# Optimization experiments

Hardware: AMD Instinct MI355X
Metric: run time of the kernel (lower is better)

Reference implementation:

```python
import jax, jax.numpy as jnp
import numpy as np

WS = 8          # window_size
NH = 8          # num_heads
D = 256         # values_dim
DQK = 128       # inner_qk_dim = int(256 * 0.5)
DV = 256        # inner_v_dim (already divisible by NH)
H1, W1 = 128, 128
H2, W2 = 192, 192
N1 = (H1 // WS) * (W1 // WS)   # 256 windows
N2 = (H2 // WS) * (W2 // WS)   # 576 windows
EPS = 1e-6


def _windows(x):
    # (B, H, W, D) -> (B, Wh*Ww, ws*ws, D)
    B, Hx, Wx, Dd = x.shape
    Wh, Ww = Hx // WS, Wx // WS
    x = x.reshape(B, Wh, WS, Ww, WS, Dd).transpose(0, 1, 3, 2, 4, 5)
    return x.reshape(B, Wh * Ww, WS * WS, Dd), (Wh, Ww)


def _unwindows(x, Wh, Ww):
    # (B, Wh*Ww, ws*ws, D) -> (B, Wh*ws, Ww*ws, D)
    B, N, n, Dd = x.shape
    x = x.reshape(B, Wh, Ww, WS, WS, Dd).transpose(0, 1, 3, 2, 4, 5)
    return x.reshape(B, Wh * WS, Ww * WS, Dd)


def _rmsnorm(x, w):
    return x * jax.lax.rsqrt(jnp.mean(x * x, axis=-1, keepdims=True) + EPS) * w


def _qkv(x, W_qk, b_qk, rms_w, W_v):
    Vw, (Wh, Ww) = _windows(x)
    B, N, n, _ = Vw.shape
    avg = Vw.mean(axis=2)                                  # (B, N, D)
    qk = _rmsnorm(avg @ W_qk + b_qk, rms_w)                # (B, N, 2*DQK)
    # 'b Wh Ww (H e) -> b H (Wh Ww) e' then chunk(2, dim=-1)
    qk = qk.reshape(B, N, NH, 2 * DQK // NH).transpose(0, 2, 1, 3)  # (B, NH, N, 32)
    q, k = jnp.split(qk, 2, axis=-1)                       # each (B, NH, N, 16)
    v = Vw @ W_v                                           # (B, N, n, DV)
    ev = DV // NH
    # 'b Wh Ww n (e H) -> b H (Wh Ww) (n e)' (head index fastest-varying in channel)
    v = v.reshape(B, N, n, ev, NH).transpose(0, 4, 1, 2, 3).reshape(B, NH, N, n * ev)
    return q, k, v, (Wh, Ww)


def reference(x1, x2, W_qk, b_qk, rms_w, W_v, W_vb):
    q1, k1, v1, s1 = _qkv(x1, W_qk, b_qk, rms_w, W_v)
    q2, k2, v2, s2 = _qkv(x2, W_qk, b_qk, rms_w, W_v)
    q = jnp.concatenate([q1, q2], axis=2)   # (B, NH, N, 16)
    k = jnp.concatenate([k1, k2], axis=2)
    v = jnp.concatenate([v1, v2], axis=2)   # (B, NH, N, n*ev)

    scale = 1.0 / jnp.sqrt(jnp.asarray(DQK, dtype=q.dtype))
    scores = jnp.einsum('bhqe,bhke->bhqk', q, k) * scale   # (B, NH, N, N)
    # block-diagonal self-source mask
    src_id = jnp.concatenate([jnp.zeros((N1,), jnp.int32), jnp.ones((N2,), jnp.int32)])
    mask = src_id[:, None] == src_id[None, :]              # (N, N) True within same source
    scores = jnp.where(mask, -jnp.inf, scores)
    A = jax.nn.softmax(scores, axis=-1)

    out = jnp.einsum('bhqk,bhkf->bhqf', A, v)              # (B, NH, N, n*ev)
    B = out.shape[0]
    n = WS * WS
    ev = DV // NH
    N = N1 + N2
    # 'b H N (n e) -> b N n (e H)'
    out = out.reshape(B, NH, N, n, ev).transpose(0, 2, 3, 4, 1).reshape(B, N, n, ev * NH)
    out = out @ W_vb                                       # (B, N, n, D)

    o1 = _unwindows(out[:, :N1], H1 // WS, W1 // WS)
    o2 = _unwindows(out[:, N1:], H2 // WS, W2 // WS)
    return (o1, o2)


def setup_inputs() -> dict:
    key = jax.random.key(0)
    ks = jax.random.split(key, 6)
    return {
        'x1': jax.random.normal(ks[0], (2, H1, W1, D), jnp.float32),
        'x2': jax.random.normal(ks[1], (2, H2, W2, D), jnp.float32),
        'W_qk': jax.random.normal(ks[2], (D, 2 * DQK), jnp.float32) * 0.02,
        'b_qk': jnp.zeros((2 * DQK,), jnp.float32),
        'rms_w': jnp.ones((2 * DQK,), jnp.float32),
        'W_v': jax.random.normal(ks[3], (D, DV), jnp.float32) * 0.02,
        'W_vb': jax.random.normal(ks[4], (DV, D), jnp.float32) * 0.02,
    }
```

## Files before the change

kernel.cpp:

```cpp
#include <hip/hip_runtime.h>

typedef __attribute__((ext_vector_type(8))) short bf16x8;
typedef __attribute__((ext_vector_type(4))) float f32x4;

#define NWIN 832
#define N1_ 256
#define N2_ 576
#define O1SZ 8388608

__device__ __forceinline__ ushort f2bf(float f) {
    union { float f; unsigned u; } v; v.f = f;
    unsigned r = v.u + 0x7fffu + ((v.u >> 16) & 1u);
    return (ushort)(r >> 16);
}

__global__ __launch_bounds__(256) void k_prep(const float* __restrict__ W_qk,
        const float* __restrict__ W_v, const float* __restrict__ W_vb,
        ushort* __restrict__ WvT, ushort* __restrict__ WvbT, float* __restrict__ WqkT)
{
    int row = blockIdx.x & 255, m = blockIdx.x >> 8, t = threadIdx.x;
    if (m == 0) {
        int j = ((row & 31) << 3) | (row >> 5);
        WvT[row * 256 + t] = f2bf(W_v[t * 256 + j]);
    } else if (m == 1) {
        WvbT[row * 256 + t] = f2bf(W_vb[t * 256 + row]);
    } else {
        WqkT[row * 256 + t] = W_qk[t * 256 + row];
    }
}

__global__ __launch_bounds__(256) void k_projv(const float* __restrict__ x1, const float* __restrict__ x2,
        const ushort* __restrict__ WvT, float* __restrict__ avg, ushort* __restrict__ vattn)
{
    __shared__ __align__(16) char smem[37888];
    ushort (*a_lds)[264] = (ushort (*)[264])smem;
    float* psumF = (float*)(smem + 33792);

    int bid = blockIdx.x, b = bid / NWIN, win = bid % NWIN;
    const float* src; int Wd, base;
    if (win < N1_) { src = x1; Wd = 128; int wh = win >> 4, ww = win & 15;
                     base = ((b*128 + wh*8)*128 + ww*8)*256; }
    else           { src = x2; Wd = 192; int w2 = win - N1_; int wh = w2/24, ww = w2%24;
                     base = ((b*192 + wh*8)*192 + ww*8)*256; }

    int t = threadIdx.x;
    int c4 = t & 63, tg = t >> 6;
    int c0 = c4 * 4;
    const float* sp = src + base + c0;
    float4 s4 = {0.f, 0.f, 0.f, 0.f};
    #pragma unroll
    for (int k = 0; k < 16; ++k) {
        int i = tg*16 + k;
        float4 g = *(const float4*)(sp + ((i>>3)*Wd + (i&7))*256);
        s4.x += g.x; s4.y += g.y; s4.z += g.z; s4.w += g.w;
        ushort4 hb = { f2bf(g.x), f2bf(g.y), f2bf(g.z), f2bf(g.w) };
        *(ushort4*)&a_lds[i][c0] = hb;
    }
    *(float4*)&psumF[tg*256 + c0] = s4;
    __syncthreads();

    {
        float a = psumF[t] + psumF[256 + t] + psumF[512 + t] + psumF[768 + t];
        avg[(b*NWIN + win)*256 + t] = a * 0.015625f;
    }

    int lane = t & 63, wv = t >> 6, lr = lane & 15, lg = lane >> 4;
    f32x4 acc[4][4];
    #pragma unroll
    for (int mt=0;mt<4;++mt)
      #pragma unroll
      for (int nt=0;nt<4;++nt) acc[mt][nt] = (f32x4){0.f,0.f,0.f,0.f};

    #pragma unroll 2
    for (int ks = 0; ks < 8; ++ks) {
        bf16x8 af[4], bfr[4];
        #pragma unroll
        for (int mt=0;mt<4;++mt) af[mt] = *(const bf16x8*)&a_lds[mt*16 + lr][ks*32 + lg*8];
        #pragma unroll
        for (int nt=0;nt<4;++nt) bfr[nt] = *(const bf16x8*)&WvT[(wv*64 + nt*16 + lr)*256 + ks*32 + lg*8];
        #pragma unroll
        for (int mt=0;mt<4;++mt)
          #pragma unroll
          for (int nt=0;nt<4;++nt)
            acc[mt][nt] = __builtin_amdgcn_mfma_f32_16x16x32_bf16(af[mt], bfr[nt], acc[mt][nt], 0, 0, 0);
    }

    __syncthreads();
    ushort (*sw)[72] = (ushort (*)[72])(smem + wv*9216);

    #pragma unroll
    for (int nt=0; nt<4; ++nt) {
        int c = nt*16 + lr;
        #pragma unroll
        for (int mt=0; mt<4; ++mt) {
            ushort4 hb = { f2bf(acc[mt][nt][0]), f2bf(acc[mt][nt][1]),
                           f2bf(acc[mt][nt][2]), f2bf(acc[mt][nt][3]) };
            *(ushort4*)&sw[c][mt*16 + lg*4] = hb;
        }
    }
    #pragma unroll
    for (int u=0; u<2; ++u) {
        int h = wv*2 + u;
        ushort* dst = &vattn[((size_t)(b*8 + h)*NWIN + win)*2048];
        #pragma unroll
        for (int it=0; it<4; ++it) {
            int q = it*64 + lane;
            int e = q >> 3, i8 = (q & 7) * 8;
            *(uint4*)&dst[e*64 + i8] = *(const uint4*)&sw[u*32 + e][i8];
        }
    }
}

__global__ __launch_bounds__(256) void k_qk(const float* __restrict__ avg, const float* __restrict__ WqkT,
        const float* __restrict__ b_qk, const float* __restrict__ rms_w,
        float* __restrict__ qv, float* __restrict__ kv)
{
    __shared__ float arow[256];
    __shared__ float red[256];
    int row = blockIdx.x, c = threadIdx.x;
    arow[c] = avg[row*256 + c];
    __syncthreads();
    const float4* wr = (const float4*)&WqkT[c*256];
    float t = 0.f;
    #pragma unroll 8
    for (int k4 = 0; k4 < 64; ++k4) {
        float4 w = wr[k4];
        t += arow[k4*4]*w.x + arow[k4*4+1]*w.y + arow[k4*4+2]*w.z + arow[k4*4+3]*w.w;
    }
    t += b_qk[c];
    red[c] = t*t;
    __syncthreads();
    for (int s = 128; s; s >>= 1) { if (c < s) red[c] += red[c+s]; __syncthreads(); }
    float ms = red[0] * (1.f/256.f);
    float y = t * rsqrtf(ms + 1e-6f) * rms_w[c];
    int b = row / NWIN, win = row % NWIN;
    int h = c >> 5, sub = c & 31;
    size_t ob = ((size_t)(b*8 + h)*NWIN + win)*16 + (sub & 15);
    if (sub < 16) qv[ob] = y; else kv[ob] = y;
}

__global__ __launch_bounds__(256) void k_sm(const float* __restrict__ qv, const float* __restrict__ kv,
        ushort* __restrict__ Amat)
{
    __shared__ float red[256];
    int rowid = blockIdx.x;
    int qg = rowid % NWIN, bh = rowid / NWIN;
    bool s1 = qg < N1_;
    int Nk = s1 ? N2_ : N1_;
    int kbase = s1 ? N1_ : 0;
    size_t Abase = (size_t)bh*294912 + (s1 ? (size_t)qg*576 : (147456 + (size_t)(qg - N1_)*256));
    const float4* qp = (const float4*)&qv[((size_t)bh*NWIN + qg)*16];
    float4 q0 = qp[0], q1 = qp[1], q2 = qp[2], q3 = qp[3];
    const float* kp = &kv[((size_t)bh*NWIN + kbase)*16];
    int t = threadIdx.x;
    float sc[3];
    #pragma unroll
    for (int it = 0; it < 3; ++it) {
        int kk = t + it*256;
        sc[it] = -1e30f;
        if (kk < Nk) {
            const float4* kr = (const float4*)&kp[(size_t)kk*16];
            float4 a = kr[0], bq = kr[1], cq = kr[2], dq = kr[3];
            float d = q0.x*a.x + q0.y*a.y + q0.z*a.z + q0.w*a.w
                    + q1.x*bq.x + q1.y*bq.y + q1.z*bq.z + q1.w*bq.w
                    + q2.x*cq.x + q2.y*cq.y + q2.z*cq.z + q2.w*cq.w
                    + q3.x*dq.x + q3.y*dq.y + q3.z*dq.z + q3.w*dq.w;
            sc[it] = d * 0.08838834764831845f;
        }
    }
    float m = fmaxf(fmaxf(sc[0], sc[1]), sc[2]);
    red[t] = m; __syncthreads();
    for (int s = 128; s; s >>= 1) { if (t < s) red[t] = fmaxf(red[t], red[t+s]); __syncthreads(); }
    float M = red[0];
    __syncthreads();
    float e0 = __expf(sc[0]-M), e1 = __expf(sc[1]-M), e2 = __expf(sc[2]-M);
    red[t] = e0 + e1 + e2; __syncthreads();
    for (int s = 128; s; s >>= 1) { if (t < s) red[t] += red[t+s]; __syncthreads(); }
    float inv = 1.f / red[0];
    float ex[3] = {e0, e1, e2};
    #pragma unroll
    for (int it = 0; it < 3; ++it) {
        int kk = t + it*256;
        if (kk < Nk) Amat[Abase + kk] = f2bf(ex[it]*inv);
    }
}

__global__ __launch_bounds__(256) void k_av(const ushort* __restrict__ Amat,
        const ushort* __restrict__ vattn, ushort* __restrict__ outc)
{
    __shared__ ushort a_lds[64][40];
    __shared__ ushort v_lds[256][40];
    int bid = blockIdx.x;
    int bh = bid / 104, r = bid % 104, fc = r / 13, qc = r % 13;
    int Nk, kbase, q0, qg0, Astride; size_t Abase;
    if (qc < 4) { Nk = N2_; kbase = N1_; q0 = qc*64; qg0 = q0;
                  Abase = (size_t)bh*294912 + (size_t)q0*576; Astride = 576; }
    else        { Nk = N1_; kbase = 0; q0 = (qc-4)*64; qg0 = N1_ + q0;
                  Abase = (size_t)bh*294912 + 147456 + (size_t)q0*256; Astride = 256; }
    const ushort* vbase = &vattn[((size_t)bh*NWIN + kbase)*2048 + fc*256];
    int t = threadIdx.x;
    int lane = t & 63, wv = t >> 6, lr = lane & 15, lg = lane >> 4;
    f32x4 acc[4][4];
    #pragma unroll
    for (int mt=0;mt<4;++mt)
      #pragma unroll
      for (int nt=0;nt<4;++nt) acc[mt][nt] = (f32x4){0.f,0.f,0.f,0.f};

    int nsteps = Nk >> 5;
    for (int ks = 0; ks < nsteps; ++ks) {
        __syncthreads();
        {
            int q = t >> 2, seg = t & 3;
            const ushort* gp = &Amat[Abase + (size_t)q*Astride + ks*32 + seg*8];
            *(uint4*)&a_lds[q][seg*8] = *(const uint4*)gp;
        }
        {
            int u = t & 7, rp = (t >> 3) & 15, half = t >> 7;
            int k0 = rp * 2;
            int kw = k0 ^ ((u & 3) << 3);
            const ushort* vp0 = &vbase[(size_t)(ks*32 + k0)*2048];
            const ushort* vp1 = vp0 + 2048;
            #pragma unroll
            for (int j = 0; j < 2; ++j) {
                int f0 = (u + 8*(half*2 + j)) * 8;
                uint4 d0 = *(const uint4*)&vp0[f0];
                uint4 d1 = *(const uint4*)&vp1[f0];
                const ushort* a0 = (const ushort*)&d0;
                const ushort* a1 = (const ushort*)&d1;
                #pragma unroll
                for (int jj = 0; jj < 8; ++jj) {
                    ushort2 w2 = { a0[jj], a1[jj] };
                    *(ushort2*)&v_lds[f0 + jj][kw] = w2;
                }
            }
        }
        __syncthreads();
        bf16x8 af[4];
        #pragma unroll
        for (int mt=0;mt<4;++mt) af[mt] = *(const bf16x8*)&a_lds[mt*16 + lr][lg*8];
        #pragma unroll
        for (int nt=0;nt<4;++nt) {
            int f = wv*64 + nt*16 + lr;
            int s3r = (f >> 3) & 3;
            bf16x8 bb = *(const bf16x8*)&v_lds[f][(lg ^ s3r) << 3];
            #pragma unroll
            for (int mt=0;mt<4;++mt)
                acc[mt][nt] = __builtin_amdgcn_mfma_f32_16x16x32_bf16(af[mt], bb, acc[mt][nt], 0, 0, 0);
        }
    }
    size_t ob = ((size_t)bh*NWIN + qg0)*2048 + fc*256;
    #pragma unroll
    for (int nt=0;nt<4;++nt) {
        int f = wv*64 + nt*16 + lr;
        #pragma unroll
        for (int mt=0;mt<4;++mt)
          #pragma unroll
          for (int rr=0;rr<4;++rr) {
            int q = mt*16 + lg*4 + rr;
            outc[ob + (size_t)q*2048 + f] = f2bf(acc[mt][nt][rr]);
          }
    }
}

__global__ __launch_bounds__(256) void k_out(const ushort* __restrict__ outc,
        const ushort* __restrict__ WvbT, float* __restrict__ out)
{
    __shared__ ushort a_lds[64][264];
    int bid = blockIdx.x, b = bid / NWIN, win = bid % NWIN;
    int t = threadIdx.x;
    int e = t >> 3, i0 = (t & 7) * 8;
    #pragma unroll
    for (int hg = 0; hg < 2; ++hg) {
        uint4 d[4];
        #pragma unroll
        for (int hh = 0; hh < 4; ++hh)
            d[hh] = *(const uint4*)&outc[((size_t)(b*8 + hg*4 + hh)*NWIN + win)*2048 + t*8];
        const ushort* p0 = (const ushort*)&d[0];
        const ushort* p1 = (const ushort*)&d[1];
        const ushort* p2 = (const ushort*)&d[2];
        const ushort* p3 = (const ushort*)&d[3];
        #pragma unroll
        for (int jj = 0; jj < 8; ++jj) {
            ushort4 w = { p0[jj], p1[jj], p2[jj], p3[jj] };
            *(ushort4*)&a_lds[i0 + jj][e*8 + hg*4] = w;
        }
    }
    __syncthreads();

    int lane = t & 63, wv = t >> 6, lr = lane & 15, lg = lane >> 4;
    f32x4 acc[4][4];
    #pragma unroll
    for (int mt=0;mt<4;++mt)
      #pragma unroll
      for (int nt=0;nt<4;++nt) acc[mt][nt] = (f32x4){0.f,0.f,0.f,0.f};

    #pragma unroll 2
    for (int ks = 0; ks < 8; ++ks) {
        bf16x8 af[4], bfr[4];
        #pragma unroll
        for (int mt=0;mt<4;++mt) af[mt] = *(const bf16x8*)&a_lds[mt*16 + lr][ks*32 + lg*8];
        #pragma unroll
        for (int nt=0;nt<4;++nt) bfr[nt] = *(const bf16x8*)&WvbT[(wv*64 + nt*16 + lr)*256 + ks*32 + lg*8];
        #pragma unroll
        for (int mt=0;mt<4;++mt)
          #pragma unroll
          for (int nt=0;nt<4;++nt)
            acc[mt][nt] = __builtin_amdgcn_mfma_f32_16x16x32_bf16(af[mt], bfr[nt], acc[mt][nt], 0, 0, 0);
    }

    int Wd, base;
    if (win < N1_) { Wd = 128; int wh = win >> 4, ww = win & 15;
                     base = ((b*128 + wh*8)*128 + ww*8)*256; }
    else           { Wd = 192; int w2 = win - N1_; int wh = w2/24, ww = w2%24;
                     base = O1SZ + ((b*192 + wh*8)*192 + ww*8)*256; }
    #pragma unroll
    for (int nt=0;nt<4;++nt) {
        int dcol = wv*64 + nt*16 + lr;
        #pragma unroll
        for (int mt=0;mt<4;++mt)
          #pragma unroll
          for (int rr=0;rr<4;++rr) {
            int i = mt*16 + lg*4 + rr;
            out[base + ((i>>3)*Wd + (i&7))*256 + dcol] = acc[mt][nt][rr];
          }
    }
}

extern "C" void kernel_launch(void* const* d_in, const int* in_sizes, int n_in,
                              void* d_out, int out_size, void* d_ws, size_t ws_size,
                              hipStream_t stream) {
    const float* x1    = (const float*)d_in[0];
    const float* x2    = (const float*)d_in[1];
    const float* W_qk  = (const float*)d_in[2];
    const float* b_qk  = (const float*)d_in[3];
    const float* rms_w = (const float*)d_in[4];
    const float* W_v   = (const float*)d_in[5];
    const float* W_vb  = (const float*)d_in[6];

    char* ws = (char*)d_ws;
    ushort* WvT   = (ushort*)(ws + 0);
    ushort* WvbT  = (ushort*)(ws + 131072);
    float*  WqkT  = (float*) (ws + 262144);
    float*  avg   = (float*) (ws + 524288);
    float*  qv    = (float*) (ws + 2228224);
    float*  kv    = (float*) (ws + 3080192);
    ushort* vattn = (ushort*)(ws + 3932160);
    ushort* Amat  = (ushort*)(ws + 58458112);
    ushort* outc  = (ushort*)(ws + 67895296);

    k_prep <<<768,   256, 0, stream>>>(W_qk, W_v, W_vb, WvT, WvbT, WqkT);
    k_projv<<<1664,  256, 0, stream>>>(x1, x2, WvT, avg, vattn);
    k_qk   <<<1664,  256, 0, stream>>>(avg, WqkT, b_qk, rms_w, qv, kv);
    k_sm   <<<13312, 256, 0, stream>>>(qv, kv, Amat);
    k_av   <<<1664,  256, 0, stream>>>(Amat, vattn, outc);
    k_out  <<<1664,  256, 0, stream>>>(outc, WvbT, (float*)d_out);
}
```

Baseline: 410.3 us.

## Widen projv to 512 threads with swizzled LDS and batch softmax rows per block

k_projv now runs 512 threads, with each wave owning one head's 32 output columns. Its LDS tile uses an XOR swizzle in place of padding, and the window average is computed from the bf16-rounded tile, which changes numerics slightly. The softmax kernel is split into two templated launches, one per source side. Each block stages that side's K in LDS and handles 8 query rows with one 32-lane group per row, reducing with shuffles instead of block-wide syncthreads. This cuts redundant K global reads and barrier overhead, at the cost of more register pressure and a less precise average.

```diff
diff --git a/kernel.cpp b/kernel.cpp
--- a/kernel.cpp
+++ b/kernel.cpp
@@ -29,12 +29,10 @@
     }
 }
 
-__global__ __launch_bounds__(256) void k_projv(const float* __restrict__ x1, const float* __restrict__ x2,
+__global__ __launch_bounds__(512) void k_projv(const float* __restrict__ x1, const float* __restrict__ x2,
         const ushort* __restrict__ WvT, float* __restrict__ avg, ushort* __restrict__ vattn)
 {
-    __shared__ __align__(16) char smem[37888];
-    ushort (*a_lds)[264] = (ushort (*)[264])smem;
-    float* psumF = (float*)(smem + 33792);
+    __shared__ __align__(16) char smem[32768];
 
     int bid = blockIdx.x, b = bid / NWIN, win = bid % NWIN;
     const float* src; int Wd, base;
@@ -44,70 +42,84 @@
                      base = ((b*192 + wh*8)*192 + ww*8)*256; }
 
     int t = threadIdx.x;
-    int c4 = t & 63, tg = t >> 6;
-    int c0 = c4 * 4;
+    int wv = t >> 6, lane = t & 63;
+    int c0 = lane * 4;
     const float* sp = src + base + c0;
-    float4 s4 = {0.f, 0.f, 0.f, 0.f};
-    #pragma unroll
-    for (int k = 0; k < 16; ++k) {
-        int i = tg*16 + k;
-        float4 g = *(const float4*)(sp + ((i>>3)*Wd + (i&7))*256);
-        s4.x += g.x; s4.y += g.y; s4.z += g.z; s4.w += g.w;
-        ushort4 hb = { f2bf(g.x), f2bf(g.y), f2bf(g.z), f2bf(g.w) };
-        *(ushort4*)&a_lds[i][c0] = hb;
-    }
-    *(float4*)&psumF[tg*256 + c0] = s4;
-    __syncthreads();
-
-    {
-        float a = psumF[t] + psumF[256 + t] + psumF[512 + t] + psumF[768 + t];
-        avg[(b*NWIN + win)*256 + t] = a * 0.015625f;
-    }
-
-    int lane = t & 63, wv = t >> 6, lr = lane & 15, lg = lane >> 4;
-    f32x4 acc[4][4];
+
+    float4 r[8];
+    #pragma unroll
+    for (int k = 0; k < 8; ++k) {
+        int i = wv*8 + k;
+        r[k] = *(const float4*)(sp + ((i>>3)*Wd + (i&7))*256);
+    }
+    #pragma unroll
+    for (int k = 0; k < 8; ++k) {
+        int i = wv*8 + k;
+        ushort4 hb = { f2bf(r[k].x), f2bf(r[k].y), f2bf(r[k].z), f2bf(r[k].w) };
+        unsigned off = (unsigned)(i*512 + c0*2) ^ ((unsigned)(i&7) << 4);
+        *(ushort4*)(smem + off) = hb;
+    }
+    __syncthreads();
+
+    if (t < 256) {
+        float s = 0.f;
+        #pragma unroll
+        for (int i = 0; i < 64; ++i) {
+            unsigned off = (unsigned)(i*512 + t*2) ^ ((unsigned)(i&7) << 4);
+            ushort u = *(const ushort*)(smem + off);
+            union { unsigned u; float f; } cv; cv.u = (unsigned)u << 16;
+            s += cv.f;
+        }
+        avg[(b*NWIN + win)*256 + t] = s * 0.015625f;
+    }
+
+    int lr = lane & 15, lg = lane >> 4;
+    unsigned axor = ((unsigned)(lr & 7)) << 4;
+    f32x4 acc[4][2];
     #pragma unroll
     for (int mt=0;mt<4;++mt)
       #pragma unroll
-      for (int nt=0;nt<4;++nt) acc[mt][nt] = (f32x4){0.f,0.f,0.f,0.f};
+      for (int nt=0;nt<2;++nt) acc[mt][nt] = (f32x4){0.f,0.f,0.f,0.f};
 
     #pragma unroll 2
     for (int ks = 0; ks < 8; ++ks) {
-        bf16x8 af[4], bfr[4];
-        #pragma unroll
-        for (int mt=0;mt<4;++mt) af[mt] = *(const bf16x8*)&a_lds[mt*16 + lr][ks*32 + lg*8];
-        #pragma unroll
-        for (int nt=0;nt<4;++nt) bfr[nt] = *(const bf16x8*)&WvT[(wv*64 + nt*16 + lr)*256 + ks*32 + lg*8];
+        bf16x8 bfr[2], af[4];
+        #pragma unroll
+        for (int nt=0;nt<2;++nt)
+            bfr[nt] = *(const bf16x8*)&WvT[(wv*32 + nt*16 + lr)*256 + ks*32 + lg*8];
+        #pragma unroll
+        for (int mt=0;mt<4;++mt) {
+            unsigned off = ((unsigned)((mt*16+lr)*512 + ks*64 + lg*16)) ^ axor;
+            af[mt] = *(const bf16x8*)(smem + off);
+        }
         #pragma unroll
         for (int mt=0;mt<4;++mt)
           #pragma unroll
-          for (int nt=0;nt<4;++nt)
+          for (int nt=0;nt<2;++nt)
             acc[mt][nt] = __builtin_amdgcn_mfma_f32_16x16x32_bf16(af[mt], bfr[nt], acc[mt][nt], 0, 0, 0);
     }
-
-    __syncthreads();
-    ushort (*sw)[72] = (ushort (*)[72])(smem + wv*9216);
-
-    #pragma unroll
-    for (int nt=0; nt<4; ++nt) {
+    __syncthreads();
+
+    char* swb = smem + wv*4096;
+    #pragma unroll
+    for (int nt=0; nt<2; ++nt) {
         int c = nt*16 + lr;
+        unsigned cx = ((unsigned)(c & 7)) << 4;
         #pragma unroll
         for (int mt=0; mt<4; ++mt) {
             ushort4 hb = { f2bf(acc[mt][nt][0]), f2bf(acc[mt][nt][1]),
                            f2bf(acc[mt][nt][2]), f2bf(acc[mt][nt][3]) };
-            *(ushort4*)&sw[c][mt*16 + lg*4] = hb;
-        }
-    }
-    #pragma unroll
-    for (int u=0; u<2; ++u) {
-        int h = wv*2 + u;
-        ushort* dst = &vattn[((size_t)(b*8 + h)*NWIN + win)*2048];
-        #pragma unroll
-        for (int it=0; it<4; ++it) {
-            int q = it*64 + lane;
-            int e = q >> 3, i8 = (q & 7) * 8;
-            *(uint4*)&dst[e*64 + i8] = *(const uint4*)&sw[u*32 + e][i8];
-        }
+            unsigned off = ((unsigned)(c*128 + (mt*16 + lg*4)*2)) ^ cx;
+            *(ushort4*)(swb + off) = hb;
+        }
+    }
+    ushort* dst = &vattn[((size_t)(b*8 + wv)*NWIN + win)*2048];
+    #pragma unroll
+    for (int it=0; it<4; ++it) {
+        int q = it*64 + lane;
+        int e = q >> 3, i0 = (q & 7) * 8;
+        unsigned off = ((unsigned)(e*128 + i0*2)) ^ (((unsigned)(e & 7)) << 4);
+        *(uint4*)&dst[e*64 + i0] = *(const uint4*)(swb + off);
     }
 }
 
@@ -139,50 +151,67 @@
     if (sub < 16) qv[ob] = y; else kv[ob] = y;
 }
 
-__global__ __launch_bounds__(256) void k_sm(const float* __restrict__ qv, const float* __restrict__ kv,
-        ushort* __restrict__ Amat)
-{
-    __shared__ float red[256];
-    int rowid = blockIdx.x;
-    int qg = rowid % NWIN, bh = rowid / NWIN;
-    bool s1 = qg < N1_;
-    int Nk = s1 ? N2_ : N1_;
-    int kbase = s1 ? N1_ : 0;
-    size_t Abase = (size_t)bh*294912 + (s1 ? (size_t)qg*576 : (147456 + (size_t)(qg - N1_)*256));
-    const float4* qp = (const float4*)&qv[((size_t)bh*NWIN + qg)*16];
-    float4 q0 = qp[0], q1 = qp[1], q2 = qp[2], q3 = qp[3];
-    const float* kp = &kv[((size_t)bh*NWIN + kbase)*16];
+template<int SIDE1>
+__global__ __launch_bounds__(256) void k_sm_t(const float* __restrict__ qv,
+        const float* __restrict__ kv, ushort* __restrict__ Amat)
+{
+    constexpr int NK    = SIDE1 ? 576 : 256;
+    constexpr int KBASE = SIDE1 ? 256 : 0;
+    constexpr int NJ    = NK / 32;
+    __shared__ __align__(16) float K_lds[NK*20];
+    __shared__ __align__(16) float q_lds[8*16];
+
+    int bid = blockIdx.x;
+    int nqc = SIDE1 ? 32 : 72;
+    int bh = bid / nqc, qc = bid % nqc;
+    int q0 = qc * 8;
+    int qgw = SIDE1 ? q0 : (N1_ + q0);
+    size_t Abase = (size_t)bh*294912 + (SIDE1 ? (size_t)q0*576 : (147456 + (size_t)q0*256));
+
     int t = threadIdx.x;
-    float sc[3];
-    #pragma unroll
-    for (int it = 0; it < 3; ++it) {
-        int kk = t + it*256;
-        sc[it] = -1e30f;
-        if (kk < Nk) {
-            const float4* kr = (const float4*)&kp[(size_t)kk*16];
-            float4 a = kr[0], bq = kr[1], cq = kr[2], dq = kr[3];
-            float d = q0.x*a.x + q0.y*a.y + q0.z*a.z + q0.w*a.w
-                    + q1.x*bq.x + q1.y*bq.y + q1.z*bq.z + q1.w*bq.w
-                    + q2.x*cq.x + q2.y*cq.y + q2.z*cq.z + q2.w*cq.w
-                    + q3.x*dq.x + q3.y*dq.y + q3.z*dq.z + q3.w*dq.w;
-            sc[it] = d * 0.08838834764831845f;
-        }
-    }
-    float m = fmaxf(fmaxf(sc[0], sc[1]), sc[2]);
-    red[t] = m; __syncthreads();
-    for (int s = 128; s; s >>= 1) { if (t < s) red[t] = fmaxf(red[t], red[t+s]); __syncthreads(); }
-    float M = red[0];
-    __syncthreads();
-    float e0 = __expf(sc[0]-M), e1 = __expf(sc[1]-M), e2 = __expf(sc[2]-M);
-    red[t] = e0 + e1 + e2; __syncthreads();
-    for (int s = 128; s; s >>= 1) { if (t < s) red[t] += red[t+s]; __syncthreads(); }
-    float inv = 1.f / red[0];
-    float ex[3] = {e0, e1, e2};
-    #pragma unroll
-    for (int it = 0; it < 3; ++it) {
-        int kk = t + it*256;
-        if (kk < Nk) Amat[Abase + kk] = f2bf(ex[it]*inv);
-    }
+    const float4* kf = (const float4*)&kv[((size_t)bh*NWIN + KBASE)*16];
+    #pragma unroll
+    for (int jj = 0; jj < (NK*4)/256; ++jj) {
+        int idx = t + jj*256;
+        float4 v = kf[idx];
+        int row = idx >> 2, piece = idx & 3;
+        *(float4*)&K_lds[row*20 + piece*4] = v;
+    }
+    if (t < 32) {
+        float4 v = ((const float4*)&qv[((size_t)bh*NWIN + qgw)*16])[t];
+        *(float4*)&q_lds[t*4] = v;
+    }
+    __syncthreads();
+
+    int rr = t >> 5, l = t & 31;
+    float q[16];
+    #pragma unroll
+    for (int c=0;c<16;++c) q[c] = q_lds[rr*16 + c];
+
+    float sc[NJ];
+    float m = -1e30f;
+    #pragma unroll
+    for (int j = 0; j < NJ; ++j) {
+        const float4* kr = (const float4*)&K_lds[(l + 32*j)*20];
+        float4 a = kr[0], bq = kr[1], cq = kr[2], dq = kr[3];
+        float d = q[0]*a.x + q[1]*a.y + q[2]*a.z + q[3]*a.w
+                + q[4]*bq.x + q[5]*bq.y + q[6]*bq.z + q[7]*bq.w
+                + q[8]*cq.x + q[9]*cq.y + q[10]*cq.z + q[11]*cq.w
+                + q[12]*dq.x + q[13]*dq.y + q[14]*dq.z + q[15]*dq.w;
+        d *= 0.08838834764831845f;
+        sc[j] = d; m = fmaxf(m, d);
+    }
+    #pragma unroll
+    for (int s = 16; s; s >>= 1) m = fmaxf(m, __shfl_xor(m, s));
+    float sum = 0.f;
+    #pragma unroll
+    for (int j = 0; j < NJ; ++j) { sc[j] = __expf(sc[j] - m); sum += sc[j]; }
+    #pragma unroll
+    for (int s = 16; s; s >>= 1) sum += __shfl_xor(sum, s);
+    float inv = 1.f / sum;
+    ushort* arow = &Amat[Abase + (size_t)rr*NK];
+    #pragma unroll
+    for (int j = 0; j < NJ; ++j) arow[l + 32*j] = f2bf(sc[j]*inv);
 }
 
 __global__ __launch_bounds__(256) void k_av(const ushort* __restrict__ Amat,
@@ -348,10 +377,11 @@
     ushort* Amat  = (ushort*)(ws + 58458112);
     ushort* outc  = (ushort*)(ws + 67895296);
 
-    k_prep <<<768,   256, 0, stream>>>(W_qk, W_v, W_vb, WvT, WvbT, WqkT);
-    k_projv<<<1664,  256, 0, stream>>>(x1, x2, WvT, avg, vattn);
-    k_qk   <<<1664,  256, 0, stream>>>(avg, WqkT, b_qk, rms_w, qv, kv);
-    k_sm   <<<13312, 256, 0, stream>>>(qv, kv, Amat);
-    k_av   <<<1664,  256, 0, stream>>>(Amat, vattn, outc);
-    k_out  <<<1664,  256, 0, stream>>>(outc, WvbT, (float*)d_out);
-}
+    k_prep   <<<768,   256, 0, stream>>>(W_qk, W_v, W_vb, WvT, WvbT, WqkT);
+    k_projv  <<<1664,  512, 0, stream>>>(x1, x2, WvT, avg, vattn);
+    k_qk     <<<1664,  256, 0, stream>>>(avg, WqkT, b_qk, rms_w, qv, kv);
+    k_sm_t<1><<<512,   256, 0, stream>>>(qv, kv, Amat);
+    k_sm_t<0><<<1152,  256, 0, stream>>>(qv, kv, Amat);
+    k_av     <<<1664,  256, 0, stream>>>(Amat, vattn, outc);
+    k_out    <<<1664,  256, 0, stream>>>(outc, WvbT, (float*)d_out);
+}
```

Result: faster. 386.9 us (-5.7%).
